# Performance work log

Measured on AMD Instinct MI355X. Metric: run time of the kernel, lower is better.

## Reference

```python
import jax, jax.numpy as jnp
from jax import lax
import numpy as np

NUM_GROUPS = 16
GN_EPS = 1e-5
POOL = 4
CLAMP_MIN, CLAMP_MAX = 0.0, 1.0


def setup_inputs() -> dict:
    key = jax.random.key(0)
    ks = jax.random.split(key, 6)
    return {
        "x": jax.random.normal(ks[0], (32, 8, 256, 256), dtype=jnp.float32),
        "conv_weight": jax.random.normal(ks[1], (64, 8, 3, 3), dtype=jnp.float32) * 0.1,
        "conv_bias": jax.random.normal(ks[2], (64,), dtype=jnp.float32) * 0.1,
        "gn_weight": jax.random.uniform(ks[3], (64,), dtype=jnp.float32, minval=0.5, maxval=1.5),
        "gn_bias": jax.random.normal(ks[4], (64,), dtype=jnp.float32) * 0.1,
        "scale": jax.random.uniform(ks[5], (64, 1, 1), dtype=jnp.float32, minval=0.5, maxval=1.5),
    }


def reference(x, conv_weight, conv_bias, gn_weight, gn_bias, scale):
    # Conv2d, stride 1, no padding: [B, 8, 256, 256] -> [B, 64, 254, 254]
    y = lax.conv_general_dilated(
        x, conv_weight, window_strides=(1, 1), padding="VALID",
        dimension_numbers=("NCHW", "OIHW", "NCHW"))
    y = y + conv_bias[None, :, None, None]

    # GroupNorm: stats over (C/G, H, W) per sample per group
    B, C, H, W = y.shape
    yg = y.reshape(B, NUM_GROUPS, -1)
    mean = jnp.mean(yg, axis=-1, keepdims=True)
    var = jnp.mean(jnp.square(yg - mean), axis=-1, keepdims=True)
    yn = ((yg - mean) * lax.rsqrt(var + GN_EPS)).reshape(B, C, H, W)
    yn = yn * gn_weight[None, :, None, None] + gn_bias[None, :, None, None]

    # Per-channel scale (shape [C,1,1] broadcasts over H,W)
    yn = yn * scale[None, :, :, :]

    # MaxPool2d(kernel=4, stride=4): [B, 64, 254, 254] -> [B, 64, 63, 63]
    p = lax.reduce_window(yn, -jnp.inf, lax.max,
                          window_dimensions=(1, 1, POOL, POOL),
                          window_strides=(1, 1, POOL, POOL),
                          padding="VALID")

    return jnp.clip(p, CLAMP_MIN, CLAMP_MAX)
```

## Files before the change

### kernel.cpp

```cpp
#include <hip/hip_runtime.h>


typedef __attribute__((ext_vector_type(8))) short bf16x8;
typedef __attribute__((ext_vector_type(16))) float f32x16;

#define NPIX 258064.0f
#define ONES_OFF 31680

__device__ __forceinline__ unsigned short f2bf_rne(float f) {
    unsigned u = __float_as_uint(f);
    u += 0x7FFFu + ((u >> 16) & 1u);
    return (unsigned short)(u >> 16);
}
__device__ __forceinline__ float bf2f(unsigned short h) {
    return __uint_as_float(((unsigned)h) << 16);
}
__device__ __forceinline__ float dppmax(float v, const int ctrl) {
    int o;
    if (ctrl == 0xB1) o = __builtin_amdgcn_mov_dpp(__float_as_int(v), 0xB1, 0xF, 0xF, true);
    else              o = __builtin_amdgcn_mov_dpp(__float_as_int(v), 0x4E, 0xF, 0xF, true);
    return fmaxf(v, __int_as_float(o));
}

__global__ __launch_bounds__(256) void prep_weights(
    const float* __restrict__ cw, const float* __restrict__ cb,
    unsigned short* __restrict__ wg)
{
    const int e = blockIdx.x * 256 + threadIdx.x;
    if (e >= 10240) return;
    const int j = e & 7, lane = (e >> 3) & 63, ot = (e >> 9) & 1;
    const int half = (e >> 10) & 1, s = e >> 11;
    const int oc = ot * 32 + (lane & 31), hh5 = lane >> 5;
    const int k = s * 16 + hh5 * 8 + j;
    float wv = 0.0f;
    if (k < 72)       wv = cw[oc * 72 + (k & 7) * 9 + (k >> 3)];
    else if (k == 72) wv = cb[oc];
    const unsigned short hi = f2bf_rne(wv);
    const unsigned short lo = f2bf_rne(wv - bf2f(hi));
    wg[e] = half ? lo : hi;
}

__global__ __launch_bounds__(256, 4) void conv_mfma(
    const float* __restrict__ x, const unsigned short* __restrict__ wg,
    float* __restrict__ pooled, float* __restrict__ stats)
{
    __shared__ __align__(16) unsigned char xs[10 * 66 * 48 + 32];

    const int tid = threadIdx.x;
    const int l = tid & 63, w = tid >> 6;
    const int ll = l & 31, hh5 = l >> 5;
    const int po = w & 1, ot = w >> 1;
    const int C0 = blockIdx.x * 64;
    const int by = blockIdx.y;
    const int R0 = by * 8;
    const int b = blockIdx.z;

    const float* xb = x + (size_t)b * 524288;
    for (int i = tid; i < 660; i += 256) {
        int row = i / 66, px = i - row * 66;
        int gr = R0 + row, gc = C0 + px;
        bool ok = (gr < 256) && (gc < 256);
        const float* p = xb + gr * 256 + gc;
        unsigned hi[4], lo[4];
        #pragma unroll
        for (int jj = 0; jj < 4; ++jj) {
            float v0 = ok ? p[(2 * jj) * 65536] : 0.0f;
            float v1 = ok ? p[(2 * jj + 1) * 65536] : 0.0f;
            unsigned short h0 = (unsigned short)(__float_as_uint(v0) >> 16);
            unsigned short h1 = (unsigned short)(__float_as_uint(v1) >> 16);
            unsigned short l0 = f2bf_rne(v0 - bf2f(h0));
            unsigned short l1 = f2bf_rne(v1 - bf2f(h1));
            hi[jj] = (unsigned)h0 | ((unsigned)h1 << 16);
            lo[jj] = (unsigned)l0 | ((unsigned)l1 << 16);
        }
        uint4* dst = (uint4*)(xs + i * 48);
        dst[0] = make_uint4(hi[0], hi[1], hi[2], hi[3]);
        dst[1] = make_uint4(lo[0], lo[1], lo[2], lo[3]);
    }
    if (tid == 0) {
        *(uint4*)(xs + ONES_OFF)      = make_uint4(0x3F80u, 0u, 0u, 0u);
        *(uint4*)(xs + ONES_OFF + 16) = make_uint4(0u, 0u, 0u, 0u);
    }
    __syncthreads();

    bf16x8 af[5][2];
    #pragma unroll
    for (int s = 0; s < 5; ++s)
        #pragma unroll
        for (int hf = 0; hf < 2; ++hf)
            af[s][hf] = *(const bf16x8*)(wg + (s * 2 + hf) * 1024 + ot * 512 + l * 8);

    const int KHe[5] = {0, 0, 1, 2, 2}, KWe[5] = {0, 2, 1, 0, 2};
    const int KHo[5] = {0, 1, 1, 2, 0}, KWo[5] = {1, 0, 2, 1, 0};
    int baseOff[5];
    #pragma unroll
    for (int s = 0; s < 5; ++s) {
        int kh = hh5 ? KHo[s] : KHe[s];
        int kw = hh5 ? KWo[s] : KWe[s];
        baseOff[s] = kh * 3168 + (po * 32 + ll + kw) * 48;
    }

    const bool pxV = (C0 + po * 32 + ll) < 254;
    const int pcol = blockIdx.x * 16 + po * 8 + (ll >> 2);
    float pm[16];
    float sacc[4] = {0.f, 0.f, 0.f, 0.f}, qacc[4] = {0.f, 0.f, 0.f, 0.f};
    #pragma unroll
    for (int j = 0; j < 16; ++j) pm[j] = -3.4e38f;

    #pragma unroll 1
    for (int r = 0; r < 8; ++r) {
        f32x16 acc;
        #pragma unroll
        for (int j = 0; j < 16; ++j) acc[j] = 0.0f;
        const unsigned char* xr = xs + r * 3168;
        #pragma unroll
        for (int s = 0; s < 5; ++s) {
            const unsigned char* bp = (s == 4 && hh5) ? (xs + ONES_OFF)
                                                      : (xr + baseOff[s]);
            bf16x8 Bh = *(const bf16x8*)bp;
            bf16x8 Bl = *(const bf16x8*)(bp + 16);
            acc = __builtin_amdgcn_mfma_f32_32x32x16_bf16(af[s][0], Bh, acc, 0, 0, 0);
            acc = __builtin_amdgcn_mfma_f32_32x32x16_bf16(af[s][1], Bh, acc, 0, 0, 0);
            acc = __builtin_amdgcn_mfma_f32_32x32x16_bf16(af[s][0], Bl, acc, 0, 0, 0);
        }
        const bool sv = ((R0 + r) < 254) && pxV;
        #pragma unroll
        for (int reg = 0; reg < 16; ++reg) {
            const float v = acc[reg];
            pm[reg] = fmaxf(pm[reg], v);
            const float vm = sv ? v : 0.0f;
            sacc[reg >> 2] += vm;
            qacc[reg >> 2] = fmaf(vm, vm, qacc[reg >> 2]);
        }
        if ((r & 3) == 3) {
            const int tY = 2 * by + (r >> 2);
            #pragma unroll
            for (int reg = 0; reg < 16; ++reg) {
                float m = dppmax(pm[reg], 0xB1);
                pm[reg] = dppmax(m, 0x4E);
            }
            if (tY < 63 && (ll & 3) == 0 && pcol < 63) {
                #pragma unroll
                for (int reg = 0; reg < 16; ++reg) {
                    int oc = ot * 32 + (reg & 3) + 8 * (reg >> 2) + 4 * hh5;
                    pooled[((b * 64 + oc) * 63 + tY) * 63 + pcol] = pm[reg];
                }
            }
            #pragma unroll
            for (int reg = 0; reg < 16; ++reg) pm[reg] = -3.4e38f;
        }
    }

    #pragma unroll
    for (int m = 1; m <= 16; m <<= 1) {
        #pragma unroll
        for (int j = 0; j < 4; ++j) {
            sacc[j] += __shfl_xor(sacc[j], m, 64);
            qacc[j] += __shfl_xor(qacc[j], m, 64);
        }
    }
    if (ll == 0) {
        #pragma unroll
        for (int j = 0; j < 4; ++j) {
            int g = ot * 8 + 2 * j + hh5;
            atomicAdd(&stats[b * 16 + g], sacc[j]);
            atomicAdd(&stats[512 + b * 16 + g], qacc[j]);
        }
    }
}

__global__ __launch_bounds__(256) void finalize_affine_clamp(
    float* __restrict__ out, const float* __restrict__ stats,
    const float* __restrict__ gnw, const float* __restrict__ gnb,
    const float* __restrict__ scale)
{
    const int bc = blockIdx.y;
    const int b = bc >> 6, c = bc & 63, g = c >> 2;
    const float sum = stats[b * 16 + g];
    const float ssq = stats[512 + b * 16 + g];
    const float invN = 1.0f / NPIX;
    const float mean = sum * invN;
    const float var  = ssq * invN - mean * mean;
    const float rs   = rsqrtf(var + 1e-5f);
    const float A  = rs * gnw[c] * scale[c];
    const float Bv = (gnb[c] - mean * rs * gnw[c]) * scale[c];
    const int base = bc * 3969;
    #pragma unroll
    for (int k = 0; k < 4; ++k) {
        int e = blockIdx.x * 1024 + k * 256 + threadIdx.x;
        if (e < 3969) {
            float v = fmaf(A, out[base + e], Bv);
            out[base + e] = fminf(fmaxf(v, 0.0f), 1.0f);
        }
    }
}

extern "C" void kernel_launch(void* const* d_in, const int* in_sizes, int n_in,
                              void* d_out, int out_size, void* d_ws, size_t ws_size,
                              hipStream_t stream) {
    const float* x     = (const float*)d_in[0];
    const float* cw    = (const float*)d_in[1];
    const float* cb    = (const float*)d_in[2];
    const float* gnw   = (const float*)d_in[3];
    const float* gnb   = (const float*)d_in[4];
    const float* scale = (const float*)d_in[5];
    float* out   = (float*)d_out;
    float* stats = (float*)d_ws;
    unsigned short* wg = (unsigned short*)((float*)d_ws + 1024);

    hipMemsetAsync(d_ws, 0, 1024 * sizeof(float), stream);

    prep_weights<<<40, 256, 0, stream>>>(cw, cb, wg);

    dim3 grid1(4, 32, 32);
    conv_mfma<<<grid1, 256, 0, stream>>>(x, wg, out, stats);

    dim3 grid2(4, 2048, 1);
    finalize_affine_clamp<<<grid2, 256, 0, stream>>>(out, stats, gnw, gnb, scale);
}
```

Measured before the change: 264.1 us.

## Interleave two conv rows per MFMA iteration, vectorize finalize, fold memset into prep

Result: faster. 256.8 us (-2.7%).

```diff
diff --git a/kernel.cpp b/kernel.cpp
--- a/kernel.cpp
+++ b/kernel.cpp
@@ -24,9 +24,10 @@
 
 __global__ __launch_bounds__(256) void prep_weights(
     const float* __restrict__ cw, const float* __restrict__ cb,
-    unsigned short* __restrict__ wg)
+    unsigned short* __restrict__ wg, float* __restrict__ stats)
 {
     const int e = blockIdx.x * 256 + threadIdx.x;
+    if (e < 1024) stats[e] = 0.0f;
     if (e >= 10240) return;
     const int j = e & 7, lane = (e >> 3) & 63, ot = (e >> 9) & 1;
     const int half = (e >> 10) & 1, s = e >> 11;
@@ -55,6 +56,13 @@
     const int R0 = by * 8;
     const int b = blockIdx.z;
 
+    bf16x8 af[5][2];
+    #pragma unroll
+    for (int s = 0; s < 5; ++s)
+        #pragma unroll
+        for (int hf = 0; hf < 2; ++hf)
+            af[s][hf] = *(const bf16x8*)(wg + (s * 2 + hf) * 1024 + ot * 512 + l * 8);
+
     const float* xb = x + (size_t)b * 524288;
     for (int i = tid; i < 660; i += 256) {
         int row = i / 66, px = i - row * 66;
@@ -83,13 +91,6 @@
     }
     __syncthreads();
 
-    bf16x8 af[5][2];
-    #pragma unroll
-    for (int s = 0; s < 5; ++s)
-        #pragma unroll
-        for (int hf = 0; hf < 2; ++hf)
-            af[s][hf] = *(const bf16x8*)(wg + (s * 2 + hf) * 1024 + ot * 512 + l * 8);
-
     const int KHe[5] = {0, 0, 1, 2, 2}, KWe[5] = {0, 2, 1, 0, 2};
     const int KHo[5] = {0, 1, 1, 2, 0}, KWo[5] = {1, 0, 2, 1, 0};
     int baseOff[5];
@@ -108,32 +109,40 @@
     for (int j = 0; j < 16; ++j) pm[j] = -3.4e38f;
 
     #pragma unroll 1
-    for (int r = 0; r < 8; ++r) {
-        f32x16 acc;
-        #pragma unroll
-        for (int j = 0; j < 16; ++j) acc[j] = 0.0f;
-        const unsigned char* xr = xs + r * 3168;
+    for (int rp = 0; rp < 4; ++rp) {
+        f32x16 accP, accQ;
+        #pragma unroll
+        for (int j = 0; j < 16; ++j) { accP[j] = 0.0f; accQ[j] = 0.0f; }
+        const unsigned char* xrP = xs + (2 * rp) * 3168;
         #pragma unroll
         for (int s = 0; s < 5; ++s) {
-            const unsigned char* bp = (s == 4 && hh5) ? (xs + ONES_OFF)
-                                                      : (xr + baseOff[s]);
-            bf16x8 Bh = *(const bf16x8*)bp;
-            bf16x8 Bl = *(const bf16x8*)(bp + 16);
-            acc = __builtin_amdgcn_mfma_f32_32x32x16_bf16(af[s][0], Bh, acc, 0, 0, 0);
-            acc = __builtin_amdgcn_mfma_f32_32x32x16_bf16(af[s][1], Bh, acc, 0, 0, 0);
-            acc = __builtin_amdgcn_mfma_f32_32x32x16_bf16(af[s][0], Bl, acc, 0, 0, 0);
-        }
-        const bool sv = ((R0 + r) < 254) && pxV;
+            const bool ones = (s == 4) && hh5;
+            const unsigned char* bpP = ones ? (xs + ONES_OFF) : (xrP + baseOff[s]);
+            const unsigned char* bpQ = ones ? (xs + ONES_OFF) : (xrP + 3168 + baseOff[s]);
+            bf16x8 BhP = *(const bf16x8*)bpP;
+            bf16x8 BlP = *(const bf16x8*)(bpP + 16);
+            bf16x8 BhQ = *(const bf16x8*)bpQ;
+            bf16x8 BlQ = *(const bf16x8*)(bpQ + 16);
+            accP = __builtin_amdgcn_mfma_f32_32x32x16_bf16(af[s][0], BhP, accP, 0, 0, 0);
+            accQ = __builtin_amdgcn_mfma_f32_32x32x16_bf16(af[s][0], BhQ, accQ, 0, 0, 0);
+            accP = __builtin_amdgcn_mfma_f32_32x32x16_bf16(af[s][1], BhP, accP, 0, 0, 0);
+            accQ = __builtin_amdgcn_mfma_f32_32x32x16_bf16(af[s][1], BhQ, accQ, 0, 0, 0);
+            accP = __builtin_amdgcn_mfma_f32_32x32x16_bf16(af[s][0], BlP, accP, 0, 0, 0);
+            accQ = __builtin_amdgcn_mfma_f32_32x32x16_bf16(af[s][0], BlQ, accQ, 0, 0, 0);
+        }
+        const bool svP = ((R0 + 2 * rp) < 254) && pxV;
+        const bool svQ = ((R0 + 2 * rp + 1) < 254) && pxV;
         #pragma unroll
         for (int reg = 0; reg < 16; ++reg) {
-            const float v = acc[reg];
-            pm[reg] = fmaxf(pm[reg], v);
-            const float vm = sv ? v : 0.0f;
-            sacc[reg >> 2] += vm;
-            qacc[reg >> 2] = fmaf(vm, vm, qacc[reg >> 2]);
-        }
-        if ((r & 3) == 3) {
-            const int tY = 2 * by + (r >> 2);
+            const float vP = accP[reg], vQ = accQ[reg];
+            pm[reg] = fmaxf(pm[reg], fmaxf(vP, vQ));
+            const float mP = svP ? vP : 0.0f;
+            const float mQ = svQ ? vQ : 0.0f;
+            sacc[reg >> 2] += mP + mQ;
+            qacc[reg >> 2] = fmaf(mP, mP, fmaf(mQ, mQ, qacc[reg >> 2]));
+        }
+        if (rp & 1) {
+            const int tY = 2 * by + (rp >> 1);
             #pragma unroll
             for (int reg = 0; reg < 16; ++reg) {
                 float m = dppmax(pm[reg], 0xB1);
@@ -174,25 +183,38 @@
     const float* __restrict__ gnw, const float* __restrict__ gnb,
     const float* __restrict__ scale)
 {
-    const int bc = blockIdx.y;
-    const int b = bc >> 6, c = bc & 63, g = c >> 2;
-    const float sum = stats[b * 16 + g];
-    const float ssq = stats[512 + b * 16 + g];
+    const int t = blockIdx.x * 256 + threadIdx.x;
+    if (t >= 2032128) return;
+    float4 v = reinterpret_cast<float4*>(out)[t];
+    float r[4] = {v.x, v.y, v.z, v.w};
+    const int I0 = t * 4;
+    const int bc0 = I0 / 3969;
+    const int bc3 = (I0 + 3) / 3969;
     const float invN = 1.0f / NPIX;
-    const float mean = sum * invN;
-    const float var  = ssq * invN - mean * mean;
-    const float rs   = rsqrtf(var + 1e-5f);
-    const float A  = rs * gnw[c] * scale[c];
-    const float Bv = (gnb[c] - mean * rs * gnw[c]) * scale[c];
-    const int base = bc * 3969;
-    #pragma unroll
-    for (int k = 0; k < 4; ++k) {
-        int e = blockIdx.x * 1024 + k * 256 + threadIdx.x;
-        if (e < 3969) {
-            float v = fmaf(A, out[base + e], Bv);
-            out[base + e] = fminf(fmaxf(v, 0.0f), 1.0f);
-        }
-    }
+    if (bc0 == bc3) {
+        const int b = bc0 >> 6, c = bc0 & 63, g = c >> 2;
+        const float mean = stats[b * 16 + g] * invN;
+        const float var  = stats[512 + b * 16 + g] * invN - mean * mean;
+        const float rs   = rsqrtf(var + 1e-5f);
+        const float A  = rs * gnw[c] * scale[c];
+        const float Bv = (gnb[c] - mean * rs * gnw[c]) * scale[c];
+        #pragma unroll
+        for (int j = 0; j < 4; ++j)
+            r[j] = fminf(fmaxf(fmaf(A, r[j], Bv), 0.0f), 1.0f);
+    } else {
+        #pragma unroll
+        for (int j = 0; j < 4; ++j) {
+            const int bc = (I0 + j) / 3969;
+            const int b = bc >> 6, c = bc & 63, g = c >> 2;
+            const float mean = stats[b * 16 + g] * invN;
+            const float var  = stats[512 + b * 16 + g] * invN - mean * mean;
+            const float rs   = rsqrtf(var + 1e-5f);
+            const float A  = rs * gnw[c] * scale[c];
+            const float Bv = (gnb[c] - mean * rs * gnw[c]) * scale[c];
+            r[j] = fminf(fmaxf(fmaf(A, r[j], Bv), 0.0f), 1.0f);
+        }
+    }
+    reinterpret_cast<float4*>(out)[t] = make_float4(r[0], r[1], r[2], r[3]);
 }
 
 extern "C" void kernel_launch(void* const* d_in, const int* in_sizes, int n_in,
@@ -208,13 +230,10 @@
     float* stats = (float*)d_ws;
     unsigned short* wg = (unsigned short*)((float*)d_ws + 1024);
 
-    hipMemsetAsync(d_ws, 0, 1024 * sizeof(float), stream);
-
-    prep_weights<<<40, 256, 0, stream>>>(cw, cb, wg);
+    prep_weights<<<40, 256, 0, stream>>>(cw, cb, wg, stats);
 
     dim3 grid1(4, 32, 32);
     conv_mfma<<<grid1, 256, 0, stream>>>(x, wg, out, stats);
 
-    dim3 grid2(4, 2048, 1);
-    finalize_affine_clamp<<<grid2, 256, 0, stream>>>(out, stats, gnw, gnb, scale);
-}
+    finalize_affine_clamp<<<(2032128 + 255) / 256, 256, 0, stream>>>(out, stats, gnw, gnb, scale);
+}
```
